# Kernel tuning notes

Hardware: AMD Instinct MI355X
Metric: run time of the kernel (lower is better)

The kernel has to match this reference:

```python
import jax, jax.numpy as jnp
import numpy as np

N_NODES = 50000
N_EDGES = 800000
N_FEAT = 128
HIDDEN = 256
N_GRAPHS = 256
N_CLASSES = 10
BN_EPS = 1e-5


def setup_inputs() -> dict:
    key = jax.random.key(0)
    ks = jax.random.split(key, 12)
    s = 1.0 / np.sqrt(HIDDEN)
    inp = {
        "x": jax.random.normal(ks[0], (N_NODES, N_FEAT), dtype=jnp.float32),
        "edge_index": jax.random.randint(ks[1], (2, N_EDGES), 0, N_NODES, dtype=jnp.int64),
        "batch": jnp.sort(jax.random.randint(ks[2], (N_NODES,), 0, N_GRAPHS, dtype=jnp.int64)),
        "conv1_w0": jax.random.normal(ks[3], (N_FEAT, HIDDEN), dtype=jnp.float32) / np.sqrt(N_FEAT),
        "conv1_b0": jnp.zeros((HIDDEN,), jnp.float32),
        "conv1_w1": jax.random.normal(ks[4], (HIDDEN, HIDDEN), dtype=jnp.float32) * s,
        "conv1_b1": jnp.zeros((HIDDEN,), jnp.float32),
        "conv1_bn_gamma": jnp.ones((HIDDEN,), jnp.float32),
        "conv1_bn_beta": jnp.zeros((HIDDEN,), jnp.float32),
        "conv1_bn_mean": jnp.zeros((HIDDEN,), jnp.float32),
        "conv1_bn_var": jnp.ones((HIDDEN,), jnp.float32),
        "convs_w0": jax.random.normal(ks[5], (3, HIDDEN, HIDDEN), dtype=jnp.float32) * s,
        "convs_b0": jnp.zeros((3, HIDDEN), jnp.float32),
        "convs_w1": jax.random.normal(ks[6], (3, HIDDEN, HIDDEN), dtype=jnp.float32) * s,
        "convs_b1": jnp.zeros((3, HIDDEN), jnp.float32),
        "convs_bn_gamma": jnp.ones((3, HIDDEN), jnp.float32),
        "convs_bn_beta": jnp.zeros((3, HIDDEN), jnp.float32),
        "convs_bn_mean": jnp.zeros((3, HIDDEN), jnp.float32),
        "convs_bn_var": jnp.ones((3, HIDDEN), jnp.float32),
        "eps": jnp.zeros((4,), jnp.float32),
        "lin1_w": jax.random.normal(ks[7], (HIDDEN, HIDDEN), dtype=jnp.float32) * s,
        "lin1_b": jnp.zeros((HIDDEN,), jnp.float32),
        "lin2_w": jax.random.normal(ks[8], (HIDDEN, N_CLASSES), dtype=jnp.float32) * s,
        "lin2_b": jnp.zeros((N_CLASSES,), jnp.float32),
    }
    return inp


def _gin_conv(x, src, dst, eps, w0, b0, w1, b1, g, be, m, v):
    # message = x[src]; aggregate = scatter_add at dst; update = MLP((1+eps)*x + aggr)
    aggr = jax.ops.segment_sum(x[src], dst, num_segments=N_NODES)
    h = (1.0 + eps) * x + aggr
    h = jax.nn.relu(h @ w0 + b0)
    h = jax.nn.relu(h @ w1 + b1)
    return (h - m) * jax.lax.rsqrt(v + BN_EPS) * g + be  # eval-mode BatchNorm1d


def reference(x, edge_index, batch,
              conv1_w0, conv1_b0, conv1_w1, conv1_b1,
              conv1_bn_gamma, conv1_bn_beta, conv1_bn_mean, conv1_bn_var,
              convs_w0, convs_b0, convs_w1, convs_b1,
              convs_bn_gamma, convs_bn_beta, convs_bn_mean, convs_bn_var,
              eps, lin1_w, lin1_b, lin2_w, lin2_b):
    src, dst = edge_index[0], edge_index[1]
    h = _gin_conv(x, src, dst, eps[0], conv1_w0, conv1_b0, conv1_w1, conv1_b1,
                  conv1_bn_gamma, conv1_bn_beta, conv1_bn_mean, conv1_bn_var)
    for i in range(convs_w0.shape[0]):
        h = _gin_conv(h, src, dst, eps[i + 1], convs_w0[i], convs_b0[i],
                      convs_w1[i], convs_b1[i], convs_bn_gamma[i], convs_bn_beta[i],
                      convs_bn_mean[i], convs_bn_var[i])
    # global_mean_pool over graph ids
    sums = jax.ops.segment_sum(h, batch, num_segments=N_GRAPHS)
    cnts = jax.ops.segment_sum(jnp.ones((N_NODES,), h.dtype), batch, num_segments=N_GRAPHS)
    pooled = sums / jnp.maximum(cnts, 1.0)[:, None]
    h = jax.nn.relu(pooled @ lin1_w + lin1_b)  # dropout is identity at inference
    logits = h @ lin2_w + lin2_b
    return jax.nn.log_softmax(logits, axis=-1)
```

## Files before the change

kernel.cpp:

```cpp
#include <hip/hip_runtime.h>
#include <hip/hip_bf16.h>

#define N_NODES 50000
#define N_EDGES 800000
#define N_FEAT 128
#define HIDDEN 256
#define N_GRAPHS 256
#define N_CLASSES 10

#define NBUCK ((N_NODES + 255) / 256)
#define EPB 2048
#define NBLK_S ((N_EDGES + EPB - 1) / EPB)

typedef __hip_bfloat16 bf16_t;
typedef short bf16x8 __attribute__((ext_vector_type(8)));
typedef float f32x4 __attribute__((ext_vector_type(4)));

__device__ inline float bfb2f(short s) {
    unsigned u = ((unsigned)(unsigned short)s) << 16;
    float f; __builtin_memcpy(&f, &u, 4); return f;
}
__device__ inline short f2bfb(float f) {
    bf16_t b = __float2bfloat16(f);
    short s; __builtin_memcpy(&s, &b, 2); return s;
}


__global__ __launch_bounds__(256) void bucket_hist_kernel(const int* __restrict__ ei,
                                                          unsigned* __restrict__ histT) {
    __shared__ unsigned lh[NBUCK];
    int t = threadIdx.x, j = blockIdx.x;
    for (int i = t; i < NBUCK; i += 256) lh[i] = 0;
    __syncthreads();
    int base = j * EPB;
    #pragma unroll
    for (int it = 0; it < EPB / 256; it++) {
        int e = base + it * 256 + t;
        if (e < N_EDGES) atomicAdd(&lh[(unsigned)ei[N_EDGES + e] >> 8], 1u);
    }
    __syncthreads();
    for (int i = t; i < NBUCK; i += 256) histT[(size_t)i * NBLK_S + j] = lh[i];
}

__global__ __launch_bounds__(256) void bucket_scan_a_kernel(unsigned* __restrict__ histT,
                                                            unsigned* __restrict__ bucketTot) {
    __shared__ unsigned tmp[256];
    int b = blockIdx.x, t = threadIdx.x;
    unsigned* row = histT + (size_t)b * NBLK_S;
    int i0 = t * 2, i1 = t * 2 + 1;
    unsigned v0 = (i0 < NBLK_S) ? row[i0] : 0u;
    unsigned v1 = (i1 < NBLK_S) ? row[i1] : 0u;
    unsigned s = v0 + v1;
    tmp[t] = s;
    __syncthreads();
    #pragma unroll
    for (int off = 1; off < 256; off <<= 1) {
        unsigned a = (t >= off) ? tmp[t - off] : 0u;
        __syncthreads();
        tmp[t] += a;
        __syncthreads();
    }
    unsigned base = tmp[t] - s;
    if (i0 < NBLK_S) row[i0] = base;
    if (i1 < NBLK_S) row[i1] = base + v0;
    if (t == 255) bucketTot[b] = tmp[255];
}

__global__ __launch_bounds__(256) void bucket_scan_b_kernel(const unsigned* __restrict__ bucketTot,
                                                            unsigned* __restrict__ bucketBase) {
    __shared__ unsigned tmp[256];
    int t = threadIdx.x;
    unsigned v = (t < NBUCK) ? bucketTot[t] : 0u;
    tmp[t] = v;
    __syncthreads();
    #pragma unroll
    for (int off = 1; off < 256; off <<= 1) {
        unsigned a = (t >= off) ? tmp[t - off] : 0u;
        __syncthreads();
        tmp[t] += a;
        __syncthreads();
    }
    if (t < NBUCK) bucketBase[t] = tmp[t] - v;
    if (t == NBUCK - 1) bucketBase[NBUCK] = tmp[t];
}

__global__ __launch_bounds__(256) void bucket_scatter_kernel(const int* __restrict__ ei,
                                                             const unsigned* __restrict__ histT,
                                                             const unsigned* __restrict__ bucketBase,
                                                             unsigned long long* __restrict__ ebuf) {
    __shared__ unsigned lcur[NBUCK];
    int t = threadIdx.x, j = blockIdx.x;
    for (int i = t; i < NBUCK; i += 256)
        lcur[i] = histT[(size_t)i * NBLK_S + j] + bucketBase[i];
    __syncthreads();
    int base = j * EPB;
    #pragma unroll
    for (int it = 0; it < EPB / 256; it++) {
        int e = base + it * 256 + t;
        if (e < N_EDGES) {
            unsigned src = (unsigned)ei[e];
            unsigned dst = (unsigned)ei[N_EDGES + e];
            unsigned pos = atomicAdd(&lcur[dst >> 8], 1u);
            ebuf[pos] = (unsigned long long)src | ((unsigned long long)dst << 32);
        }
    }
}

__global__ __launch_bounds__(256) void fine_fill_kernel(const unsigned long long* __restrict__ ebuf,
                                                        const unsigned* __restrict__ bucketBase,
                                                        unsigned* __restrict__ rowptr,
                                                        int* __restrict__ adj) {
    __shared__ unsigned ldeg[256], lcur[256], tmp[256];
    int b = blockIdx.x, t = threadIdx.x;
    unsigned sbase = bucketBase[b];
    int scnt = (int)(bucketBase[b + 1] - sbase);
    ldeg[t] = 0;
    __syncthreads();
    for (int k = t; k < scnt; k += 256) {
        unsigned dst = (unsigned)(ebuf[sbase + k] >> 32);
        atomicAdd(&ldeg[dst & 255], 1u);
    }
    __syncthreads();
    unsigned v = ldeg[t];
    tmp[t] = v;
    __syncthreads();
    for (int off = 1; off < 256; off <<= 1) {
        unsigned a = (t >= off) ? tmp[t - off] : 0u;
        __syncthreads();
        tmp[t] += a;
        __syncthreads();
    }
    unsigned exc = tmp[t] - v;
    lcur[t] = exc;
    int gnode = b * 256 + t;
    if (gnode < N_NODES) rowptr[gnode] = sbase + exc;
    if (b == NBUCK - 1 && t == 0) rowptr[N_NODES] = N_EDGES;
    __syncthreads();
    for (int k = t; k < scnt; k += 256) {
        unsigned long long p = ebuf[sbase + k];
        unsigned dst = (unsigned)(p >> 32);
        unsigned pos = atomicAdd(&lcur[dst & 255], 1u);
        adj[sbase + pos] = (int)(p & 0xffffffffu);
    }
}


__global__ __launch_bounds__(256) void convert_x_kernel(const float* __restrict__ x,
                                                        bf16_t* __restrict__ xb) {
    int i = blockIdx.x * 256 + threadIdx.x;
    if (i < N_NODES * N_FEAT / 4) {
        float4 v = reinterpret_cast<const float4*>(x)[i];
        short4 o;
        o.x = f2bfb(v.x); o.y = f2bfb(v.y); o.z = f2bfb(v.z); o.w = f2bfb(v.w);
        reinterpret_cast<short4*>(xb)[i] = o;
    }
}


__global__ __launch_bounds__(256) void prep_weights_kernel(
    const float* __restrict__ c1_w0, const float* __restrict__ c1_w1,
    const float* __restrict__ cs_w0, const float* __restrict__ cs_w1,
    bf16_t* __restrict__ wt)
{
    __shared__ float T[32][33];
    int z = blockIdx.z;
    const float* src; int K; size_t off;
    if (z == 0)      { src = c1_w0; K = N_FEAT;  off = 0; }
    else if (z == 1) { src = c1_w1; K = HIDDEN;  off = 32768; }
    else {
        int i = (z - 2) >> 1;
        src = (((z - 2) & 1) ? cs_w1 : cs_w0) + (size_t)i * HIDDEN * HIDDEN;
        K = HIDDEN;
        off = 32768 + (size_t)(z - 1) * 65536;
    }
    int k0 = blockIdx.x * 32, n0 = blockIdx.y * 32;
    if (k0 >= K) return;
    int t = threadIdx.x;
    int r = t >> 3, c4 = (t & 7) * 4;
    float4 v = *reinterpret_cast<const float4*>(src + (size_t)(k0 + r) * HIDDEN + n0 + c4);
    T[r][c4 + 0] = v.x; T[r][c4 + 1] = v.y; T[r][c4 + 2] = v.z; T[r][c4 + 3] = v.w;
    __syncthreads();
    int n = t >> 3, kc = (t & 7) * 4;
    short4 o;
    o.x = f2bfb(T[kc + 0][n]); o.y = f2bfb(T[kc + 1][n]);
    o.z = f2bfb(T[kc + 2][n]); o.w = f2bfb(T[kc + 3][n]);
    *reinterpret_cast<short4*>((short*)wt + off + (size_t)(n0 + n) * K + k0 + kc) = o;
}


__global__ __launch_bounds__(256) void aggregate1_kernel(
    const bf16_t* __restrict__ xb, const int* __restrict__ adj,
    const unsigned* __restrict__ rowptr, const float* __restrict__ eps_arr,
    bf16_t* __restrict__ out)
{
    int w = threadIdx.x >> 6, lane = threadIdx.x & 63;
    int n = blockIdx.x * 4 + w;
    if (n >= N_NODES) return;
    int q = lane >> 4, l4 = lane & 15;
    unsigned beg = rowptr[n], end = rowptr[n + 1];
    const short* xs = (const short*)xb;
    float acc[8] = {};
    unsigned e = beg;
    for (; e + 8 <= end; e += 8) {
        int s0 = adj[e + q];
        int s1 = adj[e + 4 + q];
        bf16x8 v0 = *reinterpret_cast<const bf16x8*>(xs + (unsigned)s0 * N_FEAT + l4 * 8);
        bf16x8 v1 = *reinterpret_cast<const bf16x8*>(xs + (unsigned)s1 * N_FEAT + l4 * 8);
        #pragma unroll
        for (int j = 0; j < 8; j++) acc[j] += bfb2f(v0[j]) + bfb2f(v1[j]);
    }
    for (; e + 4 <= end; e += 4) {
        int s0 = adj[e + q];
        bf16x8 v0 = *reinterpret_cast<const bf16x8*>(xs + (unsigned)s0 * N_FEAT + l4 * 8);
        #pragma unroll
        for (int j = 0; j < 8; j++) acc[j] += bfb2f(v0[j]);
    }
    int rem = (int)(end - e);
    if (q < rem) {
        bf16x8 v0 = *reinterpret_cast<const bf16x8*>(xs + (unsigned)adj[e + q] * N_FEAT + l4 * 8);
        #pragma unroll
        for (int j = 0; j < 8; j++) acc[j] += bfb2f(v0[j]);
    }
    if (q == 0) {
        bf16x8 sv = *reinterpret_cast<const bf16x8*>(xs + (unsigned)n * N_FEAT + l4 * 8);
        float ep = 1.f + eps_arr[0];
        #pragma unroll
        for (int j = 0; j < 8; j++) acc[j] += ep * bfb2f(sv[j]);
    }
    #pragma unroll
    for (int j = 0; j < 8; j++) {
        acc[j] += __shfl_xor(acc[j], 16);
        acc[j] += __shfl_xor(acc[j], 32);
    }
    if (lane < 16) {
        bf16x8 o;
        #pragma unroll
        for (int j = 0; j < 8; j++) o[j] = f2bfb(acc[j]);
        *reinterpret_cast<bf16x8*>((short*)out + (unsigned)n * N_FEAT + l4 * 8) = o;
    }
}


__global__ __launch_bounds__(256) void aggregate2_kernel(
    const bf16_t* __restrict__ x, const int* __restrict__ adj,
    const unsigned* __restrict__ rowptr, const float* __restrict__ eps_arr, int eps_idx,
    bf16_t* __restrict__ out)
{
    int w = threadIdx.x >> 6, lane = threadIdx.x & 63;
    int n = blockIdx.x * 4 + w;
    if (n >= N_NODES) return;
    int half = lane >> 5, l5 = lane & 31;
    unsigned beg = rowptr[n], end = rowptr[n + 1];
    const short* xs = (const short*)x;
    float acc[8] = {};
    unsigned e = beg;
    for (; e + 8 <= end; e += 8) {
        int s0 = adj[e + half];
        int s1 = adj[e + 2 + half];
        int s2 = adj[e + 4 + half];
        int s3 = adj[e + 6 + half];
        bf16x8 v0 = *reinterpret_cast<const bf16x8*>(xs + (unsigned)s0 * HIDDEN + l5 * 8);
        bf16x8 v1 = *reinterpret_cast<const bf16x8*>(xs + (unsigned)s1 * HIDDEN + l5 * 8);
        bf16x8 v2 = *reinterpret_cast<const bf16x8*>(xs + (unsigned)s2 * HIDDEN + l5 * 8);
        bf16x8 v3 = *reinterpret_cast<const bf16x8*>(xs + (unsigned)s3 * HIDDEN + l5 * 8);
        #pragma unroll
        for (int j = 0; j < 8; j++)
            acc[j] += (bfb2f(v0[j]) + bfb2f(v1[j])) + (bfb2f(v2[j]) + bfb2f(v3[j]));
    }
    for (; e + 2 <= end; e += 2) {
        int s0 = adj[e + half];
        bf16x8 v0 = *reinterpret_cast<const bf16x8*>(xs + (unsigned)s0 * HIDDEN + l5 * 8);
        #pragma unroll
        for (int j = 0; j < 8; j++) acc[j] += bfb2f(v0[j]);
    }
    if (e < end && half == 0) {
        bf16x8 v0 = *reinterpret_cast<const bf16x8*>(xs + (unsigned)adj[e] * HIDDEN + l5 * 8);
        #pragma unroll
        for (int j = 0; j < 8; j++) acc[j] += bfb2f(v0[j]);
    }
    if (half == 0) {
        bf16x8 sv = *reinterpret_cast<const bf16x8*>(xs + (unsigned)n * HIDDEN + l5 * 8);
        float ep = 1.f + eps_arr[eps_idx];
        #pragma unroll
        for (int j = 0; j < 8; j++) acc[j] += ep * bfb2f(sv[j]);
    }
    #pragma unroll
    for (int j = 0; j < 8; j++) acc[j] += __shfl_xor(acc[j], 32);
    if (half == 0) {
        bf16x8 o;
        #pragma unroll
        for (int j = 0; j < 8; j++) o[j] = f2bfb(acc[j]);
        *reinterpret_cast<bf16x8*>((short*)out + (unsigned)n * HIDDEN + l5 * 8) = o;
    }
}


#define GBM 128
#define GBN 128
#define GBK 64

__global__ __launch_bounds__(512) void gemm_bf16_kernel(
    const bf16_t* __restrict__ A, const bf16_t* __restrict__ Wt,
    const float* __restrict__ bias, bf16_t* __restrict__ C,
    int M, int K,
    const float* __restrict__ bn_g, const float* __restrict__ bn_b,
    const float* __restrict__ bn_m, const float* __restrict__ bn_v, int do_bn)
{
    __shared__ short lds[18432];
    short (*As)[72] = reinterpret_cast<short(*)[72]>(lds);
    short (*Bs)[72] = reinterpret_cast<short(*)[72]>(lds + 9216);
    short (*Cs)[136] = reinterpret_cast<short(*)[136]>(lds);

    int tid = threadIdx.x;
    int lane = tid & 63;
    int wave = tid >> 6;
    int wr = wave >> 2, wc = wave & 3;
    int row0 = blockIdx.x * GBM, col0 = blockIdx.y * GBN;

    int lrow = tid >> 3, lch = tid & 7;

    const short* Ab = (const short*)A;
    const short* Wb = (const short*)Wt;

    f32x4 acc[4][2] = {};

    for (int k0 = 0; k0 < K; k0 += GBK) {
        #pragma unroll
        for (int rr = 0; rr < 2; rr++) {
            int r = lrow + rr * 64;
            int arow = row0 + r;
            bf16x8 av = {};
            if (arow < M)
                av = *reinterpret_cast<const bf16x8*>(Ab + (size_t)arow * K + k0 + lch * 8);
            *reinterpret_cast<bf16x8*>(&As[r][lch * 8]) = av;
            bf16x8 bv = *reinterpret_cast<const bf16x8*>(Wb + (size_t)(col0 + r) * K + k0 + lch * 8);
            *reinterpret_cast<bf16x8*>(&Bs[r][lch * 8]) = bv;
        }
        __syncthreads();

        int fr = lane & 15, fk = (lane >> 4) * 8;
        #pragma unroll
        for (int ks = 0; ks < 2; ks++) {
            bf16x8 a[4], b[2];
            #pragma unroll
            for (int m = 0; m < 4; m++)
                a[m] = *reinterpret_cast<const bf16x8*>(&As[wr * 64 + m * 16 + fr][ks * 32 + fk]);
            #pragma unroll
            for (int n = 0; n < 2; n++)
                b[n] = *reinterpret_cast<const bf16x8*>(&Bs[wc * 32 + n * 16 + fr][ks * 32 + fk]);
            #pragma unroll
            for (int m = 0; m < 4; m++)
                #pragma unroll
                for (int n = 0; n < 2; n++)
                    acc[m][n] = __builtin_amdgcn_mfma_f32_16x16x32_bf16(a[m], b[n], acc[m][n], 0, 0, 0);
        }
        __syncthreads();
    }

    #pragma unroll
    for (int m = 0; m < 4; m++) {
        #pragma unroll
        for (int n = 0; n < 2; n++) {
            int rl = wr * 64 + m * 16 + (lane >> 4) * 4;
            int cl = wc * 32 + n * 16 + (lane & 15);
            int c = col0 + cl;
            float bi = bias[c];
            #pragma unroll
            for (int r = 0; r < 4; r++) {
                float v = acc[m][n][r] + bi;
                v = fmaxf(v, 0.f);
                if (do_bn) v = (v - bn_m[c]) * rsqrtf(bn_v[c] + 1e-5f) * bn_g[c] + bn_b[c];
                Cs[rl + r][cl] = f2bfb(v);
            }
        }
    }
    __syncthreads();
    int lr = tid >> 2, c16 = tid & 3;
    int r = row0 + lr;
    if (r < M) {
        short* Cb = (short*)C;
        #pragma unroll
        for (int cc = 0; cc < 4; cc++) {
            int ch = c16 + cc * 4;
            bf16x8 cv = *reinterpret_cast<const bf16x8*>(&Cs[lr][ch * 8]);
            *reinterpret_cast<bf16x8*>(Cb + (size_t)r * HIDDEN + col0 + ch * 8) = cv;
        }
    }
}


__global__ __launch_bounds__(256) void pool_kernel(const bf16_t* __restrict__ h,
                                                   const int* __restrict__ batch,
                                                   float* __restrict__ pooled) {
    __shared__ int sbs[2];
    __shared__ float red[4][HIDDEN];
    int g = blockIdx.x;
    if (threadIdx.x == 0) {
        int lo = 0, hi = N_NODES;
        while (lo < hi) { int mid = (lo + hi) >> 1; if (batch[mid] < g) lo = mid + 1; else hi = mid; }
        sbs[0] = lo;
        hi = N_NODES;
        while (lo < hi) { int mid = (lo + hi) >> 1; if (batch[mid] < g + 1) lo = mid + 1; else hi = mid; }
        sbs[1] = lo;
    }
    __syncthreads();
    int sbeg = sbs[0], send = sbs[1];
    int w = threadIdx.x >> 6, lane = threadIdx.x & 63;
    int half = lane >> 5, l5 = lane & 31;
    const short* hb = (const short*)h;
    float acc[8] = {};
    for (int n = sbeg + w * 2 + half; n < send; n += 8) {
        bf16x8 v = *reinterpret_cast<const bf16x8*>(hb + (size_t)n * HIDDEN + l5 * 8);
        #pragma unroll
        for (int j = 0; j < 8; j++) acc[j] += bfb2f(v[j]);
    }
    #pragma unroll
    for (int j = 0; j < 8; j++) acc[j] += __shfl_xor(acc[j], 32);
    if (half == 0) {
        #pragma unroll
        for (int j = 0; j < 8; j++) red[w][l5 * 8 + j] = acc[j];
    }
    __syncthreads();
    int t = threadIdx.x;
    float s = red[0][t] + red[1][t] + red[2][t] + red[3][t];
    float cnt = (float)(send - sbeg);
    pooled[g * HIDDEN + t] = s / fmaxf(cnt, 1.f);
}


__global__ void head_kernel(const float* __restrict__ pooled,
                            const float* __restrict__ w1, const float* __restrict__ b1,
                            const float* __restrict__ w2, const float* __restrict__ b2,
                            float* __restrict__ out) {
    int g = blockIdx.x, t = threadIdx.x;
    __shared__ float p[HIDDEN];
    __shared__ float h1[HIDDEN];
    __shared__ float lg[N_CLASSES];
    p[t] = pooled[g * HIDDEN + t];
    __syncthreads();
    float acc = b1[t];
    for (int k = 0; k < HIDDEN; k++) acc += p[k] * w1[k * HIDDEN + t];
    h1[t] = fmaxf(acc, 0.f);
    __syncthreads();
    if (t < N_CLASSES) {
        float a = b2[t];
        for (int k = 0; k < HIDDEN; k++) a += h1[k] * w2[k * N_CLASSES + t];
        lg[t] = a;
    }
    __syncthreads();
    if (t == 0) {
        float mx = lg[0];
        for (int j = 1; j < N_CLASSES; j++) mx = fmaxf(mx, lg[j]);
        float se = 0.f;
        for (int j = 0; j < N_CLASSES; j++) se += expf(lg[j] - mx);
        float lse = mx + logf(se);
        for (int j = 0; j < N_CLASSES; j++) out[g * N_CLASSES + j] = lg[j] - lse;
    }
}


extern "C" void kernel_launch(void* const* d_in, const int* in_sizes, int n_in,
                              void* d_out, int out_size, void* d_ws, size_t ws_size,
                              hipStream_t stream) {
    const float* x       = (const float*)d_in[0];
    const int*   ei      = (const int*)d_in[1];
    const int*   batch   = (const int*)d_in[2];
    const float* c1_w0   = (const float*)d_in[3];
    const float* c1_b0   = (const float*)d_in[4];
    const float* c1_w1   = (const float*)d_in[5];
    const float* c1_b1   = (const float*)d_in[6];
    const float* c1_g    = (const float*)d_in[7];
    const float* c1_be   = (const float*)d_in[8];
    const float* c1_m    = (const float*)d_in[9];
    const float* c1_v    = (const float*)d_in[10];
    const float* cs_w0   = (const float*)d_in[11];
    const float* cs_b0   = (const float*)d_in[12];
    const float* cs_w1   = (const float*)d_in[13];
    const float* cs_b1   = (const float*)d_in[14];
    const float* cs_g    = (const float*)d_in[15];
    const float* cs_be   = (const float*)d_in[16];
    const float* cs_m    = (const float*)d_in[17];
    const float* cs_v    = (const float*)d_in[18];
    const float* eps     = (const float*)d_in[19];
    const float* lin1_w  = (const float*)d_in[20];
    const float* lin1_b  = (const float*)d_in[21];
    const float* lin2_w  = (const float*)d_in[22];
    const float* lin2_b  = (const float*)d_in[23];

    char* ws = (char*)d_ws;
    size_t off = 0;
    auto alloc = [&](size_t bytes) -> void* {
        void* p = ws + off;
        off += (bytes + 255) & ~(size_t)255;
        return p;
    };

    unsigned* histT      = (unsigned*)alloc((size_t)NBUCK * NBLK_S * 4);
    unsigned* bucketTot  = (unsigned*)alloc(NBUCK * 4);
    unsigned* bucketBase = (unsigned*)alloc((NBUCK + 1) * 4);
    unsigned long long* ebuf = (unsigned long long*)alloc((size_t)N_EDGES * 8);
    unsigned* rowptr     = (unsigned*)alloc((N_NODES + 1) * 4);
    int*      adj        = (int*)alloc(N_EDGES * 4);
    bf16_t*   Wt         = (bf16_t*)alloc((size_t)(32768 + 7 * 65536) * 2);
    bf16_t*   xb         = (bf16_t*)alloc((size_t)N_NODES * N_FEAT * 2);
    bf16_t*   B1         = (bf16_t*)alloc((size_t)N_NODES * HIDDEN * 2);
    bf16_t*   B2         = (bf16_t*)alloc((size_t)N_NODES * HIDDEN * 2);
    bf16_t*   B3         = (bf16_t*)alloc((size_t)N_NODES * HIDDEN * 2);
    float*    pooled     = (float*)alloc(N_GRAPHS * HIDDEN * 4);

    bf16_t* wt_10 = Wt;
    bf16_t* wt_11 = Wt + 32768;
    auto wt_c0 = [&](int i) { return Wt + 32768 + (size_t)(1 + 2 * i) * 65536; };
    auto wt_c1 = [&](int i) { return Wt + 32768 + (size_t)(2 + 2 * i) * 65536; };

    bucket_hist_kernel<<<NBLK_S, 256, 0, stream>>>(ei, histT);
    bucket_scan_a_kernel<<<NBUCK, 256, 0, stream>>>(histT, bucketTot);
    bucket_scan_b_kernel<<<1, 256, 0, stream>>>(bucketTot, bucketBase);
    bucket_scatter_kernel<<<NBLK_S, 256, 0, stream>>>(ei, histT, bucketBase, ebuf);
    fine_fill_kernel<<<NBUCK, 256, 0, stream>>>(ebuf, bucketBase, rowptr, adj);

    convert_x_kernel<<<(N_NODES * N_FEAT / 4 + 255) / 256, 256, 0, stream>>>(x, xb);
    prep_weights_kernel<<<dim3(8, 8, 8), 256, 0, stream>>>(c1_w0, c1_w1, cs_w0, cs_w1, Wt);

    dim3 ggrid((N_NODES + GBM - 1) / GBM, HIDDEN / GBN);
    int ab = (N_NODES + 3) / 4;

    aggregate1_kernel<<<ab, 256, 0, stream>>>(xb, adj, rowptr, eps, B1);
    gemm_bf16_kernel<<<ggrid, 512, 0, stream>>>(B1, wt_10, c1_b0, B2, N_NODES, N_FEAT,
                                                nullptr, nullptr, nullptr, nullptr, 0);
    gemm_bf16_kernel<<<ggrid, 512, 0, stream>>>(B2, wt_11, c1_b1, B3, N_NODES, HIDDEN,
                                                c1_g, c1_be, c1_m, c1_v, 1);

    for (int i = 0; i < 3; i++) {
        aggregate2_kernel<<<ab, 256, 0, stream>>>(B3, adj, rowptr, eps, i + 1, B1);
        gemm_bf16_kernel<<<ggrid, 512, 0, stream>>>(B1, wt_c0(i), cs_b0 + i * HIDDEN, B2,
                                                    N_NODES, HIDDEN,
                                                    nullptr, nullptr, nullptr, nullptr, 0);
        gemm_bf16_kernel<<<ggrid, 512, 0, stream>>>(B2, wt_c1(i), cs_b1 + i * HIDDEN, B3,
                                                    N_NODES, HIDDEN,
                                                    cs_g + i * HIDDEN, cs_be + i * HIDDEN,
                                                    cs_m + i * HIDDEN, cs_v + i * HIDDEN, 1);
    }

    pool_kernel<<<N_GRAPHS, 256, 0, stream>>>(B3, batch, pooled);
    head_kernel<<<N_GRAPHS, HIDDEN, 0, stream>>>(pooled, lin1_w, lin1_b, lin2_w, lin2_b, (float*)d_out);
}
```

Baseline: 460.9 us.

## Fuse both GIN MLP GEMMs into one kernel keeping hidden tile in LDS

Replaces the pair of separate GEMM launches per conv layer with a single kernel that computes a 128-row tile through both linear layers. The intermediate activation stays in XOR-swizzled LDS instead of round-tripping through global memory, which removes the B2 buffer and half the GEMM launches. Weights are now read directly from global/L2 per wave rather than staged in LDS, and each block covers the full 256 output columns. This uses 64KB of LDS per block and more accumulator registers, which may lower occupancy.

```diff
diff --git a/kernel.cpp b/kernel.cpp
--- a/kernel.cpp
+++ b/kernel.cpp
@@ -295,95 +295,120 @@
 }
 
 
-#define GBM 128
-#define GBN 128
-#define GBK 64
-
-__global__ __launch_bounds__(512) void gemm_bf16_kernel(
-    const bf16_t* __restrict__ A, const bf16_t* __restrict__ Wt,
-    const float* __restrict__ bias, bf16_t* __restrict__ C,
-    int M, int K,
+template<int K0>
+__global__ __launch_bounds__(512) void conv_mlp_kernel(
+    const bf16_t* __restrict__ A, const bf16_t* __restrict__ W0t, const float* __restrict__ b0,
+    const bf16_t* __restrict__ W1t, const float* __restrict__ b1,
     const float* __restrict__ bn_g, const float* __restrict__ bn_b,
-    const float* __restrict__ bn_m, const float* __restrict__ bn_v, int do_bn)
+    const float* __restrict__ bn_m, const float* __restrict__ bn_v,
+    bf16_t* __restrict__ C, int M)
 {
-    __shared__ short lds[18432];
-    short (*As)[72] = reinterpret_cast<short(*)[72]>(lds);
-    short (*Bs)[72] = reinterpret_cast<short(*)[72]>(lds + 9216);
-    short (*Cs)[136] = reinterpret_cast<short(*)[136]>(lds);
-
-    int tid = threadIdx.x;
-    int lane = tid & 63;
-    int wave = tid >> 6;
+    __shared__ short sh[32768];
+    int tid = threadIdx.x, lane = tid & 63, wave = tid >> 6;
     int wr = wave >> 2, wc = wave & 3;
-    int row0 = blockIdx.x * GBM, col0 = blockIdx.y * GBN;
-
-    int lrow = tid >> 3, lch = tid & 7;
+    int row0 = blockIdx.x * 128;
+    int fr = lane & 15, fk = (lane >> 4) * 8;
 
     const short* Ab = (const short*)A;
-    const short* Wb = (const short*)Wt;
-
-    f32x4 acc[4][2] = {};
-
-    for (int k0 = 0; k0 < K; k0 += GBK) {
-        #pragma unroll
-        for (int rr = 0; rr < 2; rr++) {
-            int r = lrow + rr * 64;
-            int arow = row0 + r;
-            bf16x8 av = {};
-            if (arow < M)
-                av = *reinterpret_cast<const bf16x8*>(Ab + (size_t)arow * K + k0 + lch * 8);
-            *reinterpret_cast<bf16x8*>(&As[r][lch * 8]) = av;
-            bf16x8 bv = *reinterpret_cast<const bf16x8*>(Wb + (size_t)(col0 + r) * K + k0 + lch * 8);
-            *reinterpret_cast<bf16x8*>(&Bs[r][lch * 8]) = bv;
+    const short* W0b = (const short*)W0t;
+    const short* W1b = (const short*)W1t;
+
+    constexpr int CPR0 = K0 / 8;
+    #pragma unroll
+    for (int it = 0; it < 128 * CPR0 / 512; it++) {
+        int c = it * 512 + tid;
+        int r = c / CPR0, ch = c % CPR0;
+        int col = ch * 8;
+        bf16x8 v = {};
+        int gr = row0 + r;
+        if (gr < M) v = *reinterpret_cast<const bf16x8*>(Ab + (size_t)gr * K0 + col);
+        *reinterpret_cast<bf16x8*>(&sh[r * K0 + (col ^ ((r & 7) << 3))]) = v;
+    }
+    __syncthreads();
+
+    f32x4 acc[4][4] = {};
+    #pragma unroll
+    for (int ks = 0; ks < K0 / 32; ks++) {
+        bf16x8 a[4], b[4];
+        #pragma unroll
+        for (int m = 0; m < 4; m++) {
+            int r = wr * 64 + m * 16 + fr;
+            a[m] = *reinterpret_cast<const bf16x8*>(&sh[r * K0 + ((ks * 32 + fk) ^ ((r & 7) << 3))]);
         }
-        __syncthreads();
-
-        int fr = lane & 15, fk = (lane >> 4) * 8;
-        #pragma unroll
-        for (int ks = 0; ks < 2; ks++) {
-            bf16x8 a[4], b[2];
+        #pragma unroll
+        for (int n = 0; n < 4; n++)
+            b[n] = *reinterpret_cast<const bf16x8*>(W0b + (size_t)(wc * 64 + n * 16 + fr) * K0 + ks * 32 + fk);
+        #pragma unroll
+        for (int m = 0; m < 4; m++)
             #pragma unroll
-            for (int m = 0; m < 4; m++)
-                a[m] = *reinterpret_cast<const bf16x8*>(&As[wr * 64 + m * 16 + fr][ks * 32 + fk]);
-            #pragma unroll
-            for (int n = 0; n < 2; n++)
-                b[n] = *reinterpret_cast<const bf16x8*>(&Bs[wc * 32 + n * 16 + fr][ks * 32 + fk]);
-            #pragma unroll
-            for (int m = 0; m < 4; m++)
-                #pragma unroll
-                for (int n = 0; n < 2; n++)
-                    acc[m][n] = __builtin_amdgcn_mfma_f32_16x16x32_bf16(a[m], b[n], acc[m][n], 0, 0, 0);
-        }
-        __syncthreads();
-    }
+            for (int n = 0; n < 4; n++)
+                acc[m][n] = __builtin_amdgcn_mfma_f32_16x16x32_bf16(a[m], b[n], acc[m][n], 0, 0, 0);
+    }
+    __syncthreads();
 
     #pragma unroll
     for (int m = 0; m < 4; m++) {
-        #pragma unroll
-        for (int n = 0; n < 2; n++) {
-            int rl = wr * 64 + m * 16 + (lane >> 4) * 4;
-            int cl = wc * 32 + n * 16 + (lane & 15);
-            int c = col0 + cl;
-            float bi = bias[c];
+        int rl = wr * 64 + m * 16 + (lane >> 4) * 4;
+        #pragma unroll
+        for (int n = 0; n < 4; n++) {
+            int cl = wc * 64 + n * 16 + fr;
+            float bi = b0[cl];
             #pragma unroll
             for (int r = 0; r < 4; r++) {
-                float v = acc[m][n][r] + bi;
-                v = fmaxf(v, 0.f);
-                if (do_bn) v = (v - bn_m[c]) * rsqrtf(bn_v[c] + 1e-5f) * bn_g[c] + bn_b[c];
-                Cs[rl + r][cl] = f2bfb(v);
+                int rr = rl + r;
+                sh[rr * 256 + (cl ^ ((rr & 7) << 3))] = f2bfb(fmaxf(acc[m][n][r] + bi, 0.f));
             }
         }
     }
     __syncthreads();
-    int lr = tid >> 2, c16 = tid & 3;
-    int r = row0 + lr;
-    if (r < M) {
-        short* Cb = (short*)C;
-        #pragma unroll
-        for (int cc = 0; cc < 4; cc++) {
-            int ch = c16 + cc * 4;
-            bf16x8 cv = *reinterpret_cast<const bf16x8*>(&Cs[lr][ch * 8]);
-            *reinterpret_cast<bf16x8*>(Cb + (size_t)r * HIDDEN + col0 + ch * 8) = cv;
+
+    f32x4 acc1[4][4] = {};
+    #pragma unroll
+    for (int ks = 0; ks < 8; ks++) {
+        bf16x8 a[4], b[4];
+        #pragma unroll
+        for (int m = 0; m < 4; m++) {
+            int r = wr * 64 + m * 16 + fr;
+            a[m] = *reinterpret_cast<const bf16x8*>(&sh[r * 256 + ((ks * 32 + fk) ^ ((r & 7) << 3))]);
+        }
+        #pragma unroll
+        for (int n = 0; n < 4; n++)
+            b[n] = *reinterpret_cast<const bf16x8*>(W1b + (size_t)(wc * 64 + n * 16 + fr) * 256 + ks * 32 + fk);
+        #pragma unroll
+        for (int m = 0; m < 4; m++)
+            #pragma unroll
+            for (int n = 0; n < 4; n++)
+                acc1[m][n] = __builtin_amdgcn_mfma_f32_16x16x32_bf16(a[m], b[n], acc1[m][n], 0, 0, 0);
+    }
+    __syncthreads();
+
+    #pragma unroll
+    for (int m = 0; m < 4; m++) {
+        int rl = wr * 64 + m * 16 + (lane >> 4) * 4;
+        #pragma unroll
+        for (int n = 0; n < 4; n++) {
+            int cl = wc * 64 + n * 16 + fr;
+            float bi = b1[cl];
+            float bnm = bn_m[cl], bns = rsqrtf(bn_v[cl] + 1e-5f), bng = bn_g[cl], bnb = bn_b[cl];
+            #pragma unroll
+            for (int r = 0; r < 4; r++) {
+                int rr = rl + r;
+                float v = fmaxf(acc1[m][n][r] + bi, 0.f);
+                v = (v - bnm) * bns * bng + bnb;
+                sh[rr * 256 + (cl ^ ((rr & 7) << 3))] = f2bfb(v);
+            }
+        }
+    }
+    __syncthreads();
+    #pragma unroll
+    for (int it = 0; it < 8; it++) {
+        int c = it * 512 + tid;
+        int r = c >> 5, ch = c & 31;
+        int col = ch * 8;
+        int gr = row0 + r;
+        if (gr < M) {
+            bf16x8 v = *reinterpret_cast<const bf16x8*>(&sh[r * 256 + (col ^ ((r & 7) << 3))]);
+            *reinterpret_cast<bf16x8*>((short*)C + (size_t)gr * 256 + col) = v;
         }
     }
 }
@@ -504,7 +529,6 @@
     bf16_t*   Wt         = (bf16_t*)alloc((size_t)(32768 + 7 * 65536) * 2);
     bf16_t*   xb         = (bf16_t*)alloc((size_t)N_NODES * N_FEAT * 2);
     bf16_t*   B1         = (bf16_t*)alloc((size_t)N_NODES * HIDDEN * 2);
-    bf16_t*   B2         = (bf16_t*)alloc((size_t)N_NODES * HIDDEN * 2);
     bf16_t*   B3         = (bf16_t*)alloc((size_t)N_NODES * HIDDEN * 2);
     float*    pooled     = (float*)alloc(N_GRAPHS * HIDDEN * 4);
 
@@ -522,24 +546,20 @@
     convert_x_kernel<<<(N_NODES * N_FEAT / 4 + 255) / 256, 256, 0, stream>>>(x, xb);
     prep_weights_kernel<<<dim3(8, 8, 8), 256, 0, stream>>>(c1_w0, c1_w1, cs_w0, cs_w1, Wt);
 
-    dim3 ggrid((N_NODES + GBM - 1) / GBM, HIDDEN / GBN);
+    int cgrid = (N_NODES + 127) / 128;
     int ab = (N_NODES + 3) / 4;
 
     aggregate1_kernel<<<ab, 256, 0, stream>>>(xb, adj, rowptr, eps, B1);
-    gemm_bf16_kernel<<<ggrid, 512, 0, stream>>>(B1, wt_10, c1_b0, B2, N_NODES, N_FEAT,
-                                                nullptr, nullptr, nullptr, nullptr, 0);
-    gemm_bf16_kernel<<<ggrid, 512, 0, stream>>>(B2, wt_11, c1_b1, B3, N_NODES, HIDDEN,
-                                                c1_g, c1_be, c1_m, c1_v, 1);
+    conv_mlp_kernel<128><<<cgrid, 512, 0, stream>>>(B1, wt_10, c1_b0, wt_11, c1_b1,
+                                                    c1_g, c1_be, c1_m, c1_v, B3, N_NODES);
 
     for (int i = 0; i < 3; i++) {
         aggregate2_kernel<<<ab, 256, 0, stream>>>(B3, adj, rowptr, eps, i + 1, B1);
-        gemm_bf16_kernel<<<ggrid, 512, 0, stream>>>(B1, wt_c0(i), cs_b0 + i * HIDDEN, B2,
-                                                    N_NODES, HIDDEN,
-                                                    nullptr, nullptr, nullptr, nullptr, 0);
-        gemm_bf16_kernel<<<ggrid, 512, 0, stream>>>(B2, wt_c1(i), cs_b1 + i * HIDDEN, B3,
-                                                    N_NODES, HIDDEN,
-                                                    cs_g + i * HIDDEN, cs_be + i * HIDDEN,
-                                                    cs_m + i * HIDDEN, cs_v + i * HIDDEN, 1);
+        conv_mlp_kernel<256><<<cgrid, 512, 0, stream>>>(B1, wt_c0(i), cs_b0 + i * HIDDEN,
+                                                        wt_c1(i), cs_b1 + i * HIDDEN,
+                                                        cs_g + i * HIDDEN, cs_be + i * HIDDEN,
+                                                        cs_m + i * HIDDEN, cs_v + i * HIDDEN,
+                                                        B3, N_NODES);
     }
 
     pool_kernel<<<N_GRAPHS, 256, 0, stream>>>(B3, batch, pooled);
```

Measured after the change: 462.2 us. No clear change (+0.3%).
